# Kernel tuning notes

Measured on AMD Instinct MI355X. Metric: run time of the kernel, lower is better.

The kernel has to match this reference:

```python
import jax, jax.numpy as jnp
import numpy as np

B, S, D, H = 2, 2048, 1024, 16
HD = D // H  # head depth


def setup_inputs() -> dict:
    key = jax.random.key(0)
    ks = jax.random.split(key, 8)
    scale = 0.02
    K = jax.random.normal(ks[0], (B, S, D), jnp.float32)
    V = jax.random.normal(ks[1], (B, S, D), jnp.float32)
    Q = jax.random.normal(ks[2], (B, S, D), jnp.float32)
    # causal additive mask: 1.0 where attention is disallowed (strict upper triangle)
    mask = jnp.broadcast_to(
        jnp.triu(jnp.ones((S, S), jnp.float32), k=1)[None, None, :, :], (B, 1, S, S)
    )
    Wk = jax.random.normal(ks[3], (D, D), jnp.float32) * scale
    Wv = jax.random.normal(ks[4], (D, D), jnp.float32) * scale
    Wq = jax.random.normal(ks[5], (D, D), jnp.float32) * scale
    Wo = jax.random.normal(ks[6], (D, D), jnp.float32) * scale
    z = jnp.zeros((D,), jnp.float32)
    return {"K": K, "V": V, "Q": Q, "mask": mask,
            "Wk": Wk, "bk": z, "Wv": Wv, "bv": z,
            "Wq": Wq, "bq": z, "Wo": Wo, "bo": z}


def _split_heads(x):  # [B,S,D] -> [B,H,S,HD]
    return x.reshape(B, S, H, HD).transpose(0, 2, 1, 3)


def reference(K, V, Q, mask, Wk, bk, Wv, bv, Wq, bq, Wo, bo):
    k = _split_heads(K @ Wk + bk)
    v = _split_heads(V @ Wv + bv)
    q = _split_heads(Q @ Wq + bq)
    # NOTE: source scales by sqrt(d_model), not sqrt(head_depth)
    logits = jnp.einsum("bhqd,bhkd->bhqk", q, k) / jnp.sqrt(jnp.float32(D))
    logits = logits + mask * (-1e9)
    attn = jax.nn.softmax(logits, axis=-1)
    out = jnp.einsum("bhqk,bhkd->bhqd", attn, v)  # [B,H,S,HD]
    out = out.transpose(0, 2, 1, 3).reshape(B, S, D)
    return out @ Wo + bo
```

## Files before the change

### kernel.cpp

```cpp
#include <hip/hip_runtime.h>
#include <hip/hip_bf16.h>

typedef unsigned short u16;
typedef unsigned int u32;
typedef unsigned long long u64;
typedef __attribute__((ext_vector_type(8))) __bf16 bf16x8;
typedef __attribute__((ext_vector_type(4))) float f32x4;

#define SEQ 2048
#define DM 1024
#define NH 16
#define HDim 64

__device__ __forceinline__ float bf_lo(u32 u) { return __uint_as_float(u << 16); }
__device__ __forceinline__ float bf_hi(u32 u) { return __uint_as_float(u & 0xffff0000u); }
__device__ __forceinline__ u16 f2bf(float f) {
    u32 u = __float_as_uint(f);
    u32 r = (u + 0x7fffu + ((u >> 16) & 1u)) >> 16;
    return (u16)r;
}
__device__ __forceinline__ float bf2f(u16 h) { return __uint_as_float(((u32)h) << 16); }

#define GLD16(g, l)                                                         \
    __builtin_amdgcn_global_load_lds(                                       \
        (const __attribute__((address_space(1))) void*)(g),                 \
        (__attribute__((address_space(3))) void*)(l), 16, 0, 0)

__device__ __forceinline__ bool detect_f32(const u32* q)
{
    const u32 w = q[threadIdx.x & 63];
    const int e0 = ((w & 0xffffu) >> 7) & 0xff;
    const int e1 = (w >> 23) & 0xff;
    const unsigned long long b = __ballot(e0 >= 0x90 || e1 >= 0x90);
    return b != 0ull;
}

__global__ __launch_bounds__(256)
void prep_all(const void* __restrict__ Qin, const void* __restrict__ Kin,
              const void* __restrict__ Vin,
              const void* __restrict__ w0, const void* __restrict__ w1,
              const void* __restrict__ w2, const void* __restrict__ w3,
              const void* __restrict__ b0, const void* __restrict__ b1,
              const void* __restrict__ b2, const void* __restrict__ b3,
              u16* __restrict__ Xall, u16* __restrict__ Wtall,
              u16* __restrict__ ball)
{
    __shared__ u16 T[64 * 66];
    const bool f = detect_f32((const u32*)Qin);
    const int t = threadIdx.x;
    const int bid = blockIdx.x;

    if (bid < 6144) {
        const int z = bid >> 11;
        const int bx = bid & 2047;
        const void* src = (z == 0) ? Qin : (z == 1) ? Kin : Vin;
        const size_t i0 = ((size_t)bx * 256 + t) * 8;
        u16* d = Xall + (size_t)z * 4194304 + i0;
        if (f) {
            const uint4* s = reinterpret_cast<const uint4*>((const float*)src + i0);
            uint4 a = s[0], b = s[1];
            u16 o[8];
            o[0] = f2bf(__uint_as_float(a.x)); o[1] = f2bf(__uint_as_float(a.y));
            o[2] = f2bf(__uint_as_float(a.z)); o[3] = f2bf(__uint_as_float(a.w));
            o[4] = f2bf(__uint_as_float(b.x)); o[5] = f2bf(__uint_as_float(b.y));
            o[6] = f2bf(__uint_as_float(b.z)); o[7] = f2bf(__uint_as_float(b.w));
            *reinterpret_cast<uint4*>(d) = *reinterpret_cast<const uint4*>(o);
        } else {
            *reinterpret_cast<uint4*>(d) =
                *reinterpret_cast<const uint4*>((const u16*)src + i0);
        }
    } else if (bid < 7168) {
        const int r = bid - 6144;
        const int z = r >> 8;
        const void* src = (z == 0) ? w0 : (z == 1) ? w1 : (z == 2) ? w2 : w3;
        const int n0 = ((r >> 4) & 15) * 64;
        const int k0 = (r & 15) * 64;
        const int c = t & 63, g = t >> 6;
        if (f) {
            const float* W = (const float*)src;
#pragma unroll
            for (int i = 0; i < 16; i++) {
                const int kl = g * 16 + i;
                T[kl * 66 + c] = f2bf(W[(size_t)(k0 + kl) * DM + n0 + c]);
            }
        } else {
            const u16* W = (const u16*)src;
#pragma unroll
            for (int i = 0; i < 16; i++) {
                const int kl = g * 16 + i;
                T[kl * 66 + c] = W[(size_t)(k0 + kl) * DM + n0 + c];
            }
        }
        __syncthreads();
        u16* dst = Wtall + (size_t)z * 1048576;
#pragma unroll
        for (int i = 0; i < 16; i++) {
            const int nl = g * 16 + i;
            dst[(size_t)(n0 + nl) * DM + k0 + c] = T[c * 66 + nl];
        }
    } else {
#pragma unroll
        for (int j = 0; j < 16; j++) {
            const int idx = t * 16 + j;
            const int z = idx >> 10, e = idx & 1023;
            const void* src = (z == 0) ? b0 : (z == 1) ? b1 : (z == 2) ? b2 : b3;
            ball[idx] = f ? f2bf(((const float*)src)[e]) : ((const u16*)src)[e];
        }
    }
}

__global__ __launch_bounds__(256)
void gemm128(const u16* __restrict__ Xall, const u16* __restrict__ Wtall,
             const u16* __restrict__ ball, u16* __restrict__ Yall)
{
    __shared__ __align__(16) u16 As[128 * 32];
    __shared__ __align__(16) u16 Bs[128 * 32];

    const int zz = blockIdx.z;
    const bool swp = (zz != 2);
    const u16* X  = Xall + (size_t)zz * 4194304;
    const u16* Wt = Wtall + (size_t)zz * 1048576;

    const int t    = threadIdx.x;
    const int w    = t >> 6;
    const int lane = t & 63;
    const int quad = lane >> 4;
    const int ln   = lane & 15;
    const int m0   = blockIdx.y * 128;
    const int n0   = blockIdx.x * 128;

    f32x4 acc[4][4];
#pragma unroll
    for (int i = 0; i < 4; i++)
#pragma unroll
        for (int j = 0; j < 4; j++) acc[i][j] = (f32x4){0.f, 0.f, 0.f, 0.f};

    const u16* ag = X  + (size_t)(m0 + w * 32 + (lane >> 2)) * DM + (lane & 3) * 8;
    const u16* bg = Wt + (size_t)(n0 + w * 32 + (lane >> 2)) * DM + (lane & 3) * 8;
    u16* al = &As[w * 1024];
    u16* bl = &Bs[w * 1024];

    const int wr = (w >> 1) * 64;
    const int wc = (w & 1) * 64;

    for (int kk = 0; kk < DM; kk += 32) {
        GLD16(ag,           al);
        GLD16(ag + 16 * DM, al + 512);
        GLD16(bg,           bl);
        GLD16(bg + 16 * DM, bl + 512);
        ag += 32; bg += 32;
        __syncthreads();

        bf16x8 af[4], bfr[4];
#pragma unroll
        for (int rt = 0; rt < 4; rt++)
            af[rt] = *reinterpret_cast<const bf16x8*>(&As[(wr + rt * 16 + ln) * 32 + quad * 8]);
#pragma unroll
        for (int ct = 0; ct < 4; ct++)
            bfr[ct] = *reinterpret_cast<const bf16x8*>(&Bs[(wc + ct * 16 + ln) * 32 + quad * 8]);
        if (swp) {
#pragma unroll
            for (int rt = 0; rt < 4; rt++)
#pragma unroll
                for (int ct = 0; ct < 4; ct++)
                    acc[rt][ct] = __builtin_amdgcn_mfma_f32_16x16x32_bf16(
                        bfr[ct], af[rt], acc[rt][ct], 0, 0, 0);
        } else {
#pragma unroll
            for (int rt = 0; rt < 4; rt++)
#pragma unroll
                for (int ct = 0; ct < 4; ct++)
                    acc[rt][ct] = __builtin_amdgcn_mfma_f32_16x16x32_bf16(
                        af[rt], bfr[ct], acc[rt][ct], 0, 0, 0);
        }
        __syncthreads();
    }

    u16* Y = Yall + (size_t)zz * 4194304;

    if (swp) {
        const float scale = (zz == 0) ? 0.03125f : 1.0f;
#pragma unroll
        for (int ct = 0; ct < 4; ct++) {
            const int nb = n0 + wc + ct * 16 + quad * 4;
            const int h = nb >> 6, hd = nb & (HDim - 1);
            float bv[4];
#pragma unroll
            for (int r = 0; r < 4; r++) bv[r] = bf2f(ball[zz * 1024 + nb + r]);
#pragma unroll
            for (int rt = 0; rt < 4; rt++) {
                const int m = m0 + wr + rt * 16 + ln;
                const int b = m >> 11, s = m & (SEQ - 1);
                u16 o4[4];
#pragma unroll
                for (int r = 0; r < 4; r++)
                    o4[r] = f2bf((acc[rt][ct][r] + bv[r]) * scale);
                *reinterpret_cast<u64*>(
                    Y + (((size_t)(b * NH + h)) * SEQ + s) * HDim + hd) =
                    *reinterpret_cast<const u64*>(o4);
            }
        }
    } else {
#pragma unroll
        for (int ct = 0; ct < 4; ct++) {
            const int n = n0 + wc + ct * 16 + ln;
            const float bv = bf2f(ball[zz * 1024 + n]);
            const int h = n >> 6, hd = n & (HDim - 1);
#pragma unroll
            for (int rt = 0; rt < 4; rt++) {
                const int m = m0 + wr + rt * 16 + quad * 4;
                const int b = m >> 11, s = m & (SEQ - 1);
                u16 o4[4];
#pragma unroll
                for (int r = 0; r < 4; r++) o4[r] = f2bf(acc[rt][ct][r] + bv);
                *reinterpret_cast<u64*>(
                    Y + (((size_t)(b * NH + h) * HDim + hd) * SEQ + s)) =
                    *reinterpret_cast<const u64*>(o4);
            }
        }
    }
}

__device__ __forceinline__ void attn_tile2(
    const u16* __restrict__ Ks, const u16* __restrict__ Vs,
    u16* __restrict__ Ps, const bf16x8& qf0, const bf16x8& qf1,
    int kt, int qrow, int w, int quad, int ln, f32x4* o, float& l)
{
    f32x4 s[4];
#pragma unroll
    for (int ct = 0; ct < 4; ct++) {
        const u16* kr = &Ks[(ct * 16 + ln) * 72 + quad * 8];
        bf16x8 kf0 = *reinterpret_cast<const bf16x8*>(kr);
        bf16x8 kf1 = *reinterpret_cast<const bf16x8*>(kr + 32);
        f32x4 z = (f32x4){0.f, 0.f, 0.f, 0.f};
        z = __builtin_amdgcn_mfma_f32_16x16x32_bf16(kf0, qf0, z, 0, 0, 0);
        s[ct] = __builtin_amdgcn_mfma_f32_16x16x32_bf16(kf1, qf1, z, 0, 0, 0);
    }
#pragma unroll
    for (int ct = 0; ct < 4; ct++) {
        u16 o4[4];
#pragma unroll
        for (int r = 0; r < 4; r++) {
            const int kcol = kt * 64 + ct * 16 + quad * 4 + r;
            const float e = (kcol <= qrow) ? __expf(s[ct][r]) : 0.f;
            l += e;
            o4[r] = f2bf(e);
        }
        *reinterpret_cast<u64*>(&Ps[(w * 16 + ln) * 72 + ct * 16 + quad * 4]) =
            *reinterpret_cast<const u64*>(o4);
    }
#pragma unroll
    for (int ks = 0; ks < 2; ks++) {
        bf16x8 pf = *reinterpret_cast<const bf16x8*>(
            &Ps[(w * 16 + ln) * 72 + ks * 32 + quad * 8]);
#pragma unroll
        for (int nt = 0; nt < 4; nt++) {
            bf16x8 vf = *reinterpret_cast<const bf16x8*>(
                &Vs[(nt * 16 + ln) * 72 + ks * 32 + quad * 8]);
            o[nt] = __builtin_amdgcn_mfma_f32_16x16x32_bf16(pf, vf, o[nt], 0, 0, 0);
        }
    }
}

__global__ __launch_bounds__(256)
void attn_split(const u16* __restrict__ qh, const u16* __restrict__ kh,
                const u16* __restrict__ vt, u16* __restrict__ Opart,
                float* __restrict__ Lpart)
{
    __shared__ __align__(16) u16 Ks[64 * 72];
    __shared__ __align__(16) u16 Vs[64 * 72];
    __shared__ __align__(16) u16 Ps[64 * 72];

    const int t    = threadIdx.x;
    const int i    = blockIdx.x;
    const int bh   = blockIdx.y;
    const int c    = blockIdx.z;
    const int w    = t >> 6;
    const int lane = t & 63;
    const int quad = lane >> 4;
    const int ln   = lane & 15;
    const int qtH  = 31 - i;
    const int qtL  = i;
    const int m    = (i >= 8) ? 8 : 16 - i;
    const int kt0  = c ? m : 0;
    const int kt1  = c ? (qtH + 1) : m;

    const size_t kbase = (size_t)bh * SEQ * HDim;
    const size_t vbase = (size_t)bh * HDim * SEQ;

    const u16* qrH = qh + kbase + (size_t)(qtH * 64 + w * 16 + ln) * HDim;
    const bf16x8 qfH0 = *reinterpret_cast<const bf16x8*>(qrH + quad * 8);
    const bf16x8 qfH1 = *reinterpret_cast<const bf16x8*>(qrH + 32 + quad * 8);
    const u16* qrL = qh + kbase + (size_t)(qtL * 64 + w * 16 + ln) * HDim;
    const bf16x8 qfL0 = *reinterpret_cast<const bf16x8*>(qrL + quad * 8);
    const bf16x8 qfL1 = *reinterpret_cast<const bf16x8*>(qrL + 32 + quad * 8);

    f32x4 oH[4], oL[4];
    float lH = 0.f, lL = 0.f;
#pragma unroll
    for (int k = 0; k < 4; k++) {
        oH[k] = (f32x4){0.f, 0.f, 0.f, 0.f};
        oL[k] = (f32x4){0.f, 0.f, 0.f, 0.f};
    }

    const int srow = t >> 2;
    const int sc   = (t & 3) * 16;
    const int rowH = qtH * 64 + w * 16 + ln;
    const int rowL = qtL * 64 + w * 16 + ln;

    for (int kt = kt0; kt < kt1; kt++) {
        {
            const uint4* ks = reinterpret_cast<const uint4*>(
                kh + kbase + (size_t)(kt * 64 + srow) * HDim + sc);
            uint4* kd = reinterpret_cast<uint4*>(&Ks[srow * 72 + sc]);
            kd[0] = ks[0];
            kd[1] = ks[1];
            const uint4* vs = reinterpret_cast<const uint4*>(
                vt + vbase + (size_t)srow * SEQ + kt * 64 + sc);
            uint4* vd = reinterpret_cast<uint4*>(&Vs[srow * 72 + sc]);
            vd[0] = vs[0];
            vd[1] = vs[1];
        }
        __syncthreads();

        attn_tile2(Ks, Vs, Ps, qfH0, qfH1, kt, rowH, w, quad, ln, oH, lH);
        if (kt <= qtL)
            attn_tile2(Ks, Vs, Ps, qfL0, qfL1, kt, rowL, w, quad, ln, oL, lL);

        __syncthreads();
    }

    lH += __shfl_xor(lH, 16); lH += __shfl_xor(lH, 32);
    lL += __shfl_xor(lL, 16); lL += __shfl_xor(lL, 32);

    const size_t cb = ((size_t)c * 32 + bh) * SEQ;
    if (lane < 16) {
        Lpart[cb + qtH * 64 + w * 16 + lane] = lH;
        Lpart[cb + qtL * 64 + w * 16 + lane] = lL;
    }
#pragma unroll
    for (int r = 0; r < 4; r++) {
        const int rH = qtH * 64 + w * 16 + quad * 4 + r;
        const int rL = qtL * 64 + w * 16 + quad * 4 + r;
        u16* dH = Opart + (cb + rH) * HDim + ln;
        u16* dL = Opart + (cb + rL) * HDim + ln;
#pragma unroll
        for (int nt = 0; nt < 4; nt++) {
            dH[nt * 16] = f2bf(oH[nt][r]);
            dL[nt * 16] = f2bf(oL[nt][r]);
        }
    }
}

__global__ __launch_bounds__(256)
void attn_merge(const u16* __restrict__ Opart, const float* __restrict__ Lpart,
                u16* __restrict__ ctx)
{
    const size_t tid8 = (size_t)blockIdx.x * 256 + threadIdx.x;
    const int d8 = (int)(tid8 & 7);
    const int s  = (int)((tid8 >> 3) & (SEQ - 1));
    const int bh = (int)(tid8 >> 14);
    const size_t CSTR = (size_t)32 * SEQ * HDim;

    const uint4 a = *reinterpret_cast<const uint4*>(Opart + tid8 * 8);
    const uint4 b = *reinterpret_cast<const uint4*>(Opart + CSTR + tid8 * 8);
    const float l0 = Lpart[(size_t)bh * SEQ + s];
    const float l1 = Lpart[(size_t)32 * SEQ + (size_t)bh * SEQ + s];
    const float inv = 1.f / (l0 + l1);

    const u32 aw[4] = {a.x, a.y, a.z, a.w};
    const u32 bw[4] = {b.x, b.y, b.z, b.w};
    u32 ow[4];
#pragma unroll
    for (int p = 0; p < 4; p++) {
        const float lo = (bf_lo(aw[p]) + bf_lo(bw[p])) * inv;
        const float hi = (bf_hi(aw[p]) + bf_hi(bw[p])) * inv;
        ow[p] = (u32)f2bf(lo) | ((u32)f2bf(hi) << 16);
    }
    const int bb = bh >> 4, h = bh & 15;
    *reinterpret_cast<uint4*>(
        ctx + ((size_t)(bb * SEQ + s)) * DM + h * HDim + d8 * 8) =
        *reinterpret_cast<const uint4*>(ow);
}

__global__ __launch_bounds__(256)
void gemm_out(const u16* __restrict__ ctx, const u16* __restrict__ Wt,
              const u16* __restrict__ bias, void* __restrict__ dout,
              const u32* __restrict__ qdet)
{
    __shared__ __align__(16) u16 As[128 * 32];
    __shared__ __align__(16) u16 Bs[64 * 32];

    const int t    = threadIdx.x;
    const int w    = t >> 6;
    const int lane = t & 63;
    const int quad = lane >> 4;
    const int ln   = lane & 15;
    const int m0   = blockIdx.y * 128;
    const int n0   = blockIdx.x * 64;

    f32x4 acc[4][2];
#pragma unroll
    for (int i = 0; i < 4; i++)
#pragma unroll
        for (int j = 0; j < 2; j++) acc[i][j] = (f32x4){0.f, 0.f, 0.f, 0.f};

    const u16* ag = ctx + (size_t)(m0 + w * 32 + (lane >> 2)) * DM + (lane & 3) * 8;
    const u16* bg = Wt + (size_t)(n0 + w * 16 + (lane >> 2)) * DM + (lane & 3) * 8;
    u16* al = &As[w * 1024];
    u16* bl = &Bs[w * 512];

    const int wr = (w >> 1) * 64;
    const int wc = (w & 1) * 32;

    for (int kk = 0; kk < DM; kk += 32) {
        GLD16(ag,           al);
        GLD16(ag + 16 * DM, al + 512);
        GLD16(bg,           bl);
        ag += 32; bg += 32;
        __syncthreads();

        bf16x8 af[4], bfr[2];
#pragma unroll
        for (int rt = 0; rt < 4; rt++)
            af[rt] = *reinterpret_cast<const bf16x8*>(&As[(wr + rt * 16 + ln) * 32 + quad * 8]);
#pragma unroll
        for (int ct = 0; ct < 2; ct++)
            bfr[ct] = *reinterpret_cast<const bf16x8*>(&Bs[(wc + ct * 16 + ln) * 32 + quad * 8]);
#pragma unroll
        for (int rt = 0; rt < 4; rt++)
#pragma unroll
            for (int ct = 0; ct < 2; ct++)
                acc[rt][ct] = __builtin_amdgcn_mfma_f32_16x16x32_bf16(
                    af[rt], bfr[ct], acc[rt][ct], 0, 0, 0);
        __syncthreads();
    }

    const bool f = detect_f32(qdet);
#pragma unroll
    for (int ct = 0; ct < 2; ct++) {
        const int n = n0 + wc + ct * 16 + ln;
        const float bv = bf2f(bias[n]);
#pragma unroll
        for (int rt = 0; rt < 4; rt++) {
            const int mb = m0 + wr + rt * 16 + quad * 4;
#pragma unroll
            for (int r = 0; r < 4; r++) {
                const float val = acc[rt][ct][r] + bv;
                if (f) ((float*)dout)[(size_t)(mb + r) * DM + n] = val;
                else   ((u16*)dout)[(size_t)(mb + r) * DM + n] = f2bf(val);
            }
        }
    }
}

__global__ __launch_bounds__(64)
void detect_dtype(const u32* __restrict__ q, int* __restrict__ flag)
{
    const int t = threadIdx.x;
    const u32 w = q[t];
    const int e0 = ((w & 0xffffu) >> 7) & 0xff;
    const int e1 = (w >> 23) & 0xff;
    const unsigned long long b = __ballot(e0 >= 0x90 || e1 >= 0x90);
    if (t == 0) *flag = (b != 0ull) ? 1 : 0;
}

struct AttnAcc { f32x4 o[4]; float l[4]; };

__device__ __forceinline__ void attn_tile(
    const u16* __restrict__ Ks, const u16* __restrict__ Vs,
    u16* __restrict__ Ps, const bf16x8& qf0, const bf16x8& qf1,
    int kt, int rowb, int w, int quad, int ln, AttnAcc& a)
{
    f32x4 s[4];
#pragma unroll
    for (int ct = 0; ct < 4; ct++) {
        const u16* kr = &Ks[(ct * 16 + ln) * 72 + quad * 8];
        bf16x8 kf0 = *reinterpret_cast<const bf16x8*>(kr);
        bf16x8 kf1 = *reinterpret_cast<const bf16x8*>(kr + 32);
        f32x4 z = (f32x4){0.f, 0.f, 0.f, 0.f};
        z = __builtin_amdgcn_mfma_f32_16x16x32_bf16(qf0, kf0, z, 0, 0, 0);
        s[ct] = __builtin_amdgcn_mfma_f32_16x16x32_bf16(qf1, kf1, z, 0, 0, 0);
    }
#pragma unroll
    for (int ct = 0; ct < 4; ct++) {
        const int kcol = kt * 64 + ct * 16 + ln;
#pragma unroll
        for (int r = 0; r < 4; r++) {
            const float e = (kcol <= rowb + r) ? __expf(s[ct][r]) : 0.f;
            a.l[r] += e;
            Ps[(w * 16 + quad * 4 + r) * 68 + ct * 16 + ln] = f2bf(e);
        }
    }
#pragma unroll
    for (int ks = 0; ks < 2; ks++) {
        bf16x8 pf = *reinterpret_cast<const bf16x8*>(
            &Ps[(w * 16 + ln) * 68 + ks * 32 + quad * 8]);
#pragma unroll
        for (int nt = 0; nt < 4; nt++) {
            bf16x8 vf = *reinterpret_cast<const bf16x8*>(
                &Vs[(nt * 16 + ln) * 72 + ks * 32 + quad * 8]);
            a.o[nt] = __builtin_amdgcn_mfma_f32_16x16x32_bf16(pf, vf, a.o[nt], 0, 0, 0);
        }
    }
}

__global__ __launch_bounds__(256)
void attn_mfma(const u16* __restrict__ qh, const u16* __restrict__ kh,
               const u16* __restrict__ vt, u16* __restrict__ ctx)
{
    __shared__ __align__(16) u16 Ks[64 * 72];
    __shared__ __align__(16) u16 Vs[64 * 72];
    __shared__ __align__(16) u16 Ps[64 * 68];

    const int t    = threadIdx.x;
    const int i    = blockIdx.x;
    const int bh   = blockIdx.y;
    const int w    = t >> 6;
    const int lane = t & 63;
    const int quad = lane >> 4;
    const int ln   = lane & 15;
    const int qtH  = 31 - i;
    const int qtL  = i;

    const size_t kbase = (size_t)bh * SEQ * HDim;
    const size_t vbase = (size_t)bh * HDim * SEQ;

    const u16* qrH = qh + kbase + (size_t)(qtH * 64 + w * 16 + ln) * HDim;
    const bf16x8 qfH0 = *reinterpret_cast<const bf16x8*>(qrH + quad * 8);
    const bf16x8 qfH1 = *reinterpret_cast<const bf16x8*>(qrH + 32 + quad * 8);
    const u16* qrL = qh + kbase + (size_t)(qtL * 64 + w * 16 + ln) * HDim;
    const bf16x8 qfL0 = *reinterpret_cast<const bf16x8*>(qrL + quad * 8);
    const bf16x8 qfL1 = *reinterpret_cast<const bf16x8*>(qrL + 32 + quad * 8);

    AttnAcc aH, aL;
#pragma unroll
    for (int k = 0; k < 4; k++) {
        aH.o[k] = (f32x4){0.f, 0.f, 0.f, 0.f}; aH.l[k] = 0.f;
        aL.o[k] = (f32x4){0.f, 0.f, 0.f, 0.f}; aL.l[k] = 0.f;
    }

    const int srow = t >> 2;
    const int sc   = (t & 3) * 16;
    const int rowHb = qtH * 64 + w * 16 + quad * 4;
    const int rowLb = qtL * 64 + w * 16 + quad * 4;

    for (int kt = 0; kt <= qtH; kt++) {
        {
            const uint4* ks = reinterpret_cast<const uint4*>(
                kh + kbase + (size_t)(kt * 64 + srow) * HDim + sc);
            uint4* kd = reinterpret_cast<uint4*>(&Ks[srow * 72 + sc]);
            kd[0] = ks[0];
            kd[1] = ks[1];
            const uint4* vs = reinterpret_cast<const uint4*>(
                vt + vbase + (size_t)srow * SEQ + kt * 64 + sc);
            uint4* vd = reinterpret_cast<uint4*>(&Vs[srow * 72 + sc]);
            vd[0] = vs[0];
            vd[1] = vs[1];
        }
        __syncthreads();

        attn_tile(Ks, Vs, Ps, qfH0, qfH1, kt, rowHb, w, quad, ln, aH);
        if (kt <= qtL)
            attn_tile(Ks, Vs, Ps, qfL0, qfL1, kt, rowLb, w, quad, ln, aL);

        __syncthreads();
    }

#pragma unroll
    for (int m = 1; m < 16; m <<= 1) {
#pragma unroll
        for (int r = 0; r < 4; r++) {
            aH.l[r] += __shfl_xor(aH.l[r], m);
            aL.l[r] += __shfl_xor(aL.l[r], m);
        }
    }

    const int b = bh >> 4;
    const int h = bh & 15;
#pragma unroll
    for (int r = 0; r < 4; r++) {
        const float invH = 1.f / aH.l[r];
        const float invL = 1.f / aL.l[r];
        const int sH = qtH * 64 + w * 16 + quad * 4 + r;
        const int sL = qtL * 64 + w * 16 + quad * 4 + r;
        u16* dH = ctx + ((size_t)(b * SEQ + sH)) * DM + h * HDim + ln;
        u16* dL = ctx + ((size_t)(b * SEQ + sL)) * DM + h * HDim + ln;
#pragma unroll
        for (int nt = 0; nt < 4; nt++) {
            dH[nt * 16] = f2bf(aH.o[nt][r] * invH);
            dL[nt * 16] = f2bf(aL.o[nt][r] * invL);
        }
    }
}

__global__ __launch_bounds__(256)
void gemm_bias(const void* __restrict__ Xv, const void* __restrict__ Wv,
               const void* __restrict__ biasv, void* __restrict__ Yv,
               int M, int N, int K, int mode, int xsel, int wsel, int ysel,
               float scale, const int* __restrict__ flagp)
{
    __shared__ __align__(16) u16 As[64 * 32];
    __shared__ __align__(16) u16 Bs[64 * 40];

    const int f  = *flagp;
    const bool xf = (xsel != 0) && (f != 0);
    const bool wf = (wsel != 0) && (f != 0);
    const bool yf = (ysel != 0) && (f != 0);

    const u16*   Xb = (const u16*)Xv;
    const float* Xf = (const float*)Xv;
    const u16*   Wb = (const u16*)Wv;
    const float* Wf = (const float*)Wv;

    const int t    = threadIdx.x;
    const int m0   = blockIdx.y * 64;
    const int n0   = blockIdx.x * 64;
    const int w    = t >> 6;
    const int lane = t & 63;
    const int quad = lane >> 4;
    const int ln   = lane & 15;

    f32x4 acc[4];
#pragma unroll
    for (int i = 0; i < 4; i++) acc[i] = (f32x4){0.f, 0.f, 0.f, 0.f};

    const int a_row = t >> 2;
    const int a_c8  = (t & 3) * 8;
    const int b_n   = t & 63;
    const int b_k8  = (t >> 6) * 8;

    for (int kk = 0; kk < K; kk += 32) {
        const size_t aoff = (size_t)(m0 + a_row) * K + kk + a_c8;
        if (!xf) {
            *reinterpret_cast<uint4*>(&As[a_row * 32 + a_c8]) =
                *reinterpret_cast<const uint4*>(Xb + aoff);
        } else {
            const float* src = Xf + aoff;
            uint4 u0 = reinterpret_cast<const uint4*>(src)[0];
            uint4 u1 = reinterpret_cast<const uint4*>(src)[1];
            u16 tmp[8];
            tmp[0] = f2bf(__uint_as_float(u0.x));
            tmp[1] = f2bf(__uint_as_float(u0.y));
            tmp[2] = f2bf(__uint_as_float(u0.z));
            tmp[3] = f2bf(__uint_as_float(u0.w));
            tmp[4] = f2bf(__uint_as_float(u1.x));
            tmp[5] = f2bf(__uint_as_float(u1.y));
            tmp[6] = f2bf(__uint_as_float(u1.z));
            tmp[7] = f2bf(__uint_as_float(u1.w));
            *reinterpret_cast<uint4*>(&As[a_row * 32 + a_c8]) =
                *reinterpret_cast<const uint4*>(tmp);
        }
        u16 tmp[8];
        if (!wf) {
#pragma unroll
            for (int j = 0; j < 8; j++)
                tmp[j] = Wb[(size_t)(kk + b_k8 + j) * N + n0 + b_n];
        } else {
#pragma unroll
            for (int j = 0; j < 8; j++)
                tmp[j] = f2bf(Wf[(size_t)(kk + b_k8 + j) * N + n0 + b_n]);
        }
        *reinterpret_cast<uint4*>(&Bs[b_n * 40 + b_k8]) =
            *reinterpret_cast<const uint4*>(tmp);

        __syncthreads();

        bf16x8 bfrag = *reinterpret_cast<const bf16x8*>(&Bs[(w * 16 + ln) * 40 + quad * 8]);
#pragma unroll
        for (int rt = 0; rt < 4; rt++) {
            bf16x8 afrag = *reinterpret_cast<const bf16x8*>(&As[(rt * 16 + ln) * 32 + quad * 8]);
            acc[rt] = __builtin_amdgcn_mfma_f32_16x16x32_bf16(afrag, bfrag, acc[rt], 0, 0, 0);
        }
        __syncthreads();
    }

    const int n = n0 + w * 16 + ln;
    const float bv = wf ? ((const float*)biasv)[n] : bf2f(((const u16*)biasv)[n]);
#pragma unroll
    for (int rt = 0; rt < 4; rt++) {
        if (mode == 2) {
            const int m = m0 + rt * 16 + quad * 4;
            const int b = m >> 11;
            const int s = m & (SEQ - 1);
            const int h = n >> 6;
            const int hd = n & (HDim - 1);
            u16 o4[4];
#pragma unroll
            for (int r = 0; r < 4; r++) o4[r] = f2bf((acc[rt][r] + bv) * scale);
            *reinterpret_cast<u64*>(
                (u16*)Yv + (((size_t)(b * NH + h) * HDim + hd) * SEQ + s)) =
                *reinterpret_cast<const u64*>(o4);
        } else {
#pragma unroll
            for (int r = 0; r < 4; r++) {
                const int m = m0 + rt * 16 + quad * 4 + r;
                const float val = (acc[rt][r] + bv) * scale;
                if (mode == 0) {
                    if (yf) ((float*)Yv)[(size_t)m * N + n] = val;
                    else    ((u16*)Yv)[(size_t)m * N + n] = f2bf(val);
                } else {
                    const int b = m >> 11;
                    const int s = m & (SEQ - 1);
                    const int h = n >> 6;
                    const int hd = n & (HDim - 1);
                    ((u16*)Yv)[(((size_t)(b * NH + h)) * SEQ + s) * HDim + hd] = f2bf(val);
                }
            }
        }
    }
}

extern "C" void kernel_launch(void* const* d_in, const int* in_sizes, int n_in,
                              void* d_out, int out_size, void* d_ws, size_t ws_size,
                              hipStream_t stream)
{
    const void* Kin = d_in[0];
    const void* Vin = d_in[1];
    const void* Qin = d_in[2];
    const void* Wk = d_in[4];
    const void* bk = d_in[5];
    const void* Wv = d_in[6];
    const void* bv = d_in[7];
    const void* Wq = d_in[8];
    const void* bq = d_in[9];
    const void* Wo = d_in[10];
    const void* bo = d_in[11];

    char* ws = (char*)d_ws;
    const size_t NEED = ((size_t)29360128 + 4096) * 2 + 256;

    if (ws_size >= NEED) {
        u16* Xall  = (u16*)ws;
        u16* Yall  = (u16*)ws + 12582912;
        u16* Wtall = (u16*)ws + 25165824;
        u16* ball  = (u16*)ws + 29360128;
        u16* qhp   = Yall;
        u16* khp   = Yall + 4194304;
        u16* vtp   = Yall + 8388608;
        u16* ctx   = Xall;
        u16* Opart = Xall + 4194304;
        float* Lpart = (float*)Wtall;

        hipLaunchKernelGGL(prep_all, dim3(7169), dim3(256), 0, stream,
                           Qin, Kin, Vin, Wq, Wk, Wv, Wo, bq, bk, bv, bo,
                           Xall, Wtall, ball);

        hipLaunchKernelGGL(gemm128, dim3(8, 32, 3), dim3(256), 0, stream,
                           Xall, Wtall, ball, Yall);

        hipLaunchKernelGGL(attn_split, dim3(16, 32, 2), dim3(256), 0, stream,
                           qhp, khp, vtp, Opart, Lpart);

        hipLaunchKernelGGL(attn_merge, dim3(2048), dim3(256), 0, stream,
                           Opart, Lpart, ctx);

        hipLaunchKernelGGL(gemm_out, dim3(16, 32), dim3(256), 0, stream,
                           ctx, Wtall + (size_t)3 * 1048576, ball + 3 * 1024,
                           d_out, (const u32*)Qin);
    } else {
        const size_t SEG = (size_t)2 * SEQ * DM * sizeof(u16);
        u16* qh  = (u16*)(ws);
        u16* khd = (u16*)(ws + SEG);
        u16* vtd = (u16*)(ws + 2 * SEG);
        u16* ctx = (u16*)(ws + 3 * SEG);
        int* flag = (int*)(ws + 4 * SEG);

        hipLaunchKernelGGL(detect_dtype, dim3(1), dim3(64), 0, stream,
                           (const u32*)Qin, flag);

        const int M = 2 * SEQ;
        dim3 ggrid(DM / 64, M / 64);
        dim3 gblk(256);

        hipLaunchKernelGGL(gemm_bias, ggrid, gblk, 0, stream, Qin, Wq, bq, qh,  M, DM, DM, 1, 1, 1, 0, 0.03125f, flag);
        hipLaunchKernelGGL(gemm_bias, ggrid, gblk, 0, stream, Kin, Wk, bk, khd, M, DM, DM, 1, 1, 1, 0, 1.0f,     flag);
        hipLaunchKernelGGL(gemm_bias, ggrid, gblk, 0, stream, Vin, Wv, bv, vtd, M, DM, DM, 2, 1, 1, 0, 1.0f,     flag);

        hipLaunchKernelGGL(attn_mfma, dim3(16, 2 * NH), dim3(256), 0,
                           stream, qh, khd, vtd, ctx);

        hipLaunchKernelGGL(gemm_bias, ggrid, gblk, 0, stream, ctx, Wo, bo, d_out, M, DM, DM, 0, 0, 1, 1, 1.0f, flag);
    }
}
```

Before: 269.9 us.

## Double-buffer GEMM LDS tiles with XOR swizzle and prefetch attention K/V tiles

Both projection GEMMs and the output GEMM now use two LDS buffers, so the global-to-LDS load of the next K-slice is issued before computing on the current one, leaving one barrier per step instead of two. The global source columns and LDS read offsets are XOR-swizzled to reduce LDS bank conflicts on the fragment reads. The attention kernel prefetches the next K/V tile into registers while computing the current tile. The cost is doubled LDS use in the GEMMs and extra registers in attention, which may lower occupancy.

```diff
diff --git a/kernel.cpp b/kernel.cpp
--- a/kernel.cpp
+++ b/kernel.cpp
@@ -113,8 +113,8 @@
 void gemm128(const u16* __restrict__ Xall, const u16* __restrict__ Wtall,
              const u16* __restrict__ ball, u16* __restrict__ Yall)
 {
-    __shared__ __align__(16) u16 As[128 * 32];
-    __shared__ __align__(16) u16 Bs[128 * 32];
+    __shared__ __align__(16) u16 As[2][128 * 32];
+    __shared__ __align__(16) u16 Bs[2][128 * 32];
 
     const int zz = blockIdx.z;
     const bool swp = (zz != 2);
@@ -135,46 +135,56 @@
 #pragma unroll
         for (int j = 0; j < 4; j++) acc[i][j] = (f32x4){0.f, 0.f, 0.f, 0.f};
 
-    const u16* ag = X  + (size_t)(m0 + w * 32 + (lane >> 2)) * DM + (lane & 3) * 8;
-    const u16* bg = Wt + (size_t)(n0 + w * 32 + (lane >> 2)) * DM + (lane & 3) * 8;
-    u16* al = &As[w * 1024];
-    u16* bl = &Bs[w * 1024];
+    const int swz = (lane >> 3) & 3;
+    const u16* ag = X  + (size_t)(m0 + w * 32 + (lane >> 2)) * DM + ((lane & 3) ^ swz) * 8;
+    const u16* bg = Wt + (size_t)(n0 + w * 32 + (lane >> 2)) * DM + ((lane & 3) ^ swz) * 8;
 
     const int wr = (w >> 1) * 64;
     const int wc = (w & 1) * 64;
-
-    for (int kk = 0; kk < DM; kk += 32) {
-        GLD16(ag,           al);
-        GLD16(ag + 16 * DM, al + 512);
-        GLD16(bg,           bl);
-        GLD16(bg + 16 * DM, bl + 512);
-        ag += 32; bg += 32;
-        __syncthreads();
-
-        bf16x8 af[4], bfr[4];
-#pragma unroll
-        for (int rt = 0; rt < 4; rt++)
-            af[rt] = *reinterpret_cast<const bf16x8*>(&As[(wr + rt * 16 + ln) * 32 + quad * 8]);
-#pragma unroll
-        for (int ct = 0; ct < 4; ct++)
-            bfr[ct] = *reinterpret_cast<const bf16x8*>(&Bs[(wc + ct * 16 + ln) * 32 + quad * 8]);
-        if (swp) {
-#pragma unroll
-            for (int rt = 0; rt < 4; rt++)
-#pragma unroll
-                for (int ct = 0; ct < 4; ct++)
-                    acc[rt][ct] = __builtin_amdgcn_mfma_f32_16x16x32_bf16(
-                        bfr[ct], af[rt], acc[rt][ct], 0, 0, 0);
-        } else {
-#pragma unroll
-            for (int rt = 0; rt < 4; rt++)
-#pragma unroll
-                for (int ct = 0; ct < 4; ct++)
-                    acc[rt][ct] = __builtin_amdgcn_mfma_f32_16x16x32_bf16(
-                        af[rt], bfr[ct], acc[rt][ct], 0, 0, 0);
-        }
-        __syncthreads();
-    }
+    const int rs = (quad ^ ((ln >> 1) & 3)) * 8;
+
+#define GSTAGE(B)                                        \
+    {                                                    \
+        GLD16(ag,           &As[B][w * 1024]);           \
+        GLD16(ag + 16 * DM, &As[B][w * 1024 + 512]);     \
+        GLD16(bg,           &Bs[B][w * 1024]);           \
+        GLD16(bg + 16 * DM, &Bs[B][w * 1024 + 512]);     \
+        ag += 32; bg += 32;                              \
+    }
+
+#define GCOMP(B)                                                              \
+    {                                                                         \
+        bf16x8 af[4], bfr[4];                                                 \
+        _Pragma("unroll") for (int rt = 0; rt < 4; rt++)                      \
+            af[rt] = *reinterpret_cast<const bf16x8*>(                        \
+                &As[B][(wr + rt * 16 + ln) * 32 + rs]);                       \
+        _Pragma("unroll") for (int ct = 0; ct < 4; ct++)                      \
+            bfr[ct] = *reinterpret_cast<const bf16x8*>(                       \
+                &Bs[B][(wc + ct * 16 + ln) * 32 + rs]);                       \
+        if (swp) {                                                            \
+            _Pragma("unroll") for (int rt = 0; rt < 4; rt++)                  \
+                _Pragma("unroll") for (int ct = 0; ct < 4; ct++)              \
+                    acc[rt][ct] = __builtin_amdgcn_mfma_f32_16x16x32_bf16(    \
+                        bfr[ct], af[rt], acc[rt][ct], 0, 0, 0);               \
+        } else {                                                              \
+            _Pragma("unroll") for (int rt = 0; rt < 4; rt++)                  \
+                _Pragma("unroll") for (int ct = 0; ct < 4; ct++)              \
+                    acc[rt][ct] = __builtin_amdgcn_mfma_f32_16x16x32_bf16(    \
+                        af[rt], bfr[ct], acc[rt][ct], 0, 0, 0);               \
+        }                                                                     \
+    }
+
+    GSTAGE(0);
+    __syncthreads();
+#pragma unroll 1
+    for (int it = 0; it < 15; ++it) {
+        GSTAGE(1); GCOMP(0); __syncthreads();
+        GSTAGE(0); GCOMP(1); __syncthreads();
+    }
+    GSTAGE(1); GCOMP(0); __syncthreads();
+    GCOMP(1);
+#undef GSTAGE
+#undef GCOMP
 
     u16* Y = Yall + (size_t)zz * 4194304;
 
@@ -308,20 +318,34 @@
     const int rowH = qtH * 64 + w * 16 + ln;
     const int rowL = qtL * 64 + w * 16 + ln;
 
+    uint4 kr0, kr1, vr0, vr1;
+    {
+        const uint4* ksp = reinterpret_cast<const uint4*>(
+            kh + kbase + (size_t)(kt0 * 64 + srow) * HDim + sc);
+        kr0 = ksp[0]; kr1 = ksp[1];
+        const uint4* vsp = reinterpret_cast<const uint4*>(
+            vt + vbase + (size_t)srow * SEQ + kt0 * 64 + sc);
+        vr0 = vsp[0]; vr1 = vsp[1];
+    }
+
     for (int kt = kt0; kt < kt1; kt++) {
         {
-            const uint4* ks = reinterpret_cast<const uint4*>(
-                kh + kbase + (size_t)(kt * 64 + srow) * HDim + sc);
             uint4* kd = reinterpret_cast<uint4*>(&Ks[srow * 72 + sc]);
-            kd[0] = ks[0];
-            kd[1] = ks[1];
-            const uint4* vs = reinterpret_cast<const uint4*>(
-                vt + vbase + (size_t)srow * SEQ + kt * 64 + sc);
+            kd[0] = kr0; kd[1] = kr1;
             uint4* vd = reinterpret_cast<uint4*>(&Vs[srow * 72 + sc]);
-            vd[0] = vs[0];
-            vd[1] = vs[1];
+            vd[0] = vr0; vd[1] = vr1;
         }
         __syncthreads();
+
+        if (kt + 1 < kt1) {
+            const uint4* ksp = reinterpret_cast<const uint4*>(
+                kh + kbase + (size_t)((kt + 1) * 64 + srow) * HDim + sc);
+            kr0 = ksp[0]; kr1 = ksp[1];
+            const uint4* vsp = reinterpret_cast<const uint4*>(
+                vt + vbase + (size_t)srow * SEQ + (kt + 1) * 64 + sc);
+            vr0 = vsp[0]; vr1 = vsp[1];
+            __builtin_amdgcn_sched_barrier(0);
+        }
 
         attn_tile2(Ks, Vs, Ps, qfH0, qfH1, kt, rowH, w, quad, ln, oH, lH);
         if (kt <= qtL)
@@ -388,8 +412,8 @@
               const u16* __restrict__ bias, void* __restrict__ dout,
               const u32* __restrict__ qdet)
 {
-    __shared__ __align__(16) u16 As[128 * 32];
-    __shared__ __align__(16) u16 Bs[64 * 32];
+    __shared__ __align__(16) u16 As[2][128 * 32];
+    __shared__ __align__(16) u16 Bs[2][64 * 32];
 
     const int t    = threadIdx.x;
     const int w    = t >> 6;
@@ -405,36 +429,48 @@
 #pragma unroll
         for (int j = 0; j < 2; j++) acc[i][j] = (f32x4){0.f, 0.f, 0.f, 0.f};
 
-    const u16* ag = ctx + (size_t)(m0 + w * 32 + (lane >> 2)) * DM + (lane & 3) * 8;
-    const u16* bg = Wt + (size_t)(n0 + w * 16 + (lane >> 2)) * DM + (lane & 3) * 8;
-    u16* al = &As[w * 1024];
-    u16* bl = &Bs[w * 512];
+    const int swz = (lane >> 3) & 3;
+    const u16* ag = ctx + (size_t)(m0 + w * 32 + (lane >> 2)) * DM + ((lane & 3) ^ swz) * 8;
+    const u16* bg = Wt + (size_t)(n0 + w * 16 + (lane >> 2)) * DM + ((lane & 3) ^ swz) * 8;
 
     const int wr = (w >> 1) * 64;
     const int wc = (w & 1) * 32;
-
-    for (int kk = 0; kk < DM; kk += 32) {
-        GLD16(ag,           al);
-        GLD16(ag + 16 * DM, al + 512);
-        GLD16(bg,           bl);
-        ag += 32; bg += 32;
-        __syncthreads();
-
-        bf16x8 af[4], bfr[2];
-#pragma unroll
-        for (int rt = 0; rt < 4; rt++)
-            af[rt] = *reinterpret_cast<const bf16x8*>(&As[(wr + rt * 16 + ln) * 32 + quad * 8]);
-#pragma unroll
-        for (int ct = 0; ct < 2; ct++)
-            bfr[ct] = *reinterpret_cast<const bf16x8*>(&Bs[(wc + ct * 16 + ln) * 32 + quad * 8]);
-#pragma unroll
-        for (int rt = 0; rt < 4; rt++)
-#pragma unroll
-            for (int ct = 0; ct < 2; ct++)
-                acc[rt][ct] = __builtin_amdgcn_mfma_f32_16x16x32_bf16(
-                    af[rt], bfr[ct], acc[rt][ct], 0, 0, 0);
-        __syncthreads();
-    }
+    const int rs = (quad ^ ((ln >> 1) & 3)) * 8;
+
+#define OSTAGE(B)                                        \
+    {                                                    \
+        GLD16(ag,           &As[B][w * 1024]);           \
+        GLD16(ag + 16 * DM, &As[B][w * 1024 + 512]);     \
+        GLD16(bg,           &Bs[B][w * 512]);            \
+        ag += 32; bg += 32;                              \
+    }
+
+#define OCOMP(B)                                                              \
+    {                                                                         \
+        bf16x8 af[4], bfr[2];                                                 \
+        _Pragma("unroll") for (int rt = 0; rt < 4; rt++)                      \
+            af[rt] = *reinterpret_cast<const bf16x8*>(                        \
+                &As[B][(wr + rt * 16 + ln) * 32 + rs]);                       \
+        _Pragma("unroll") for (int ct = 0; ct < 2; ct++)                      \
+            bfr[ct] = *reinterpret_cast<const bf16x8*>(                       \
+                &Bs[B][(wc + ct * 16 + ln) * 32 + rs]);                       \
+        _Pragma("unroll") for (int rt = 0; rt < 4; rt++)                      \
+            _Pragma("unroll") for (int ct = 0; ct < 2; ct++)                  \
+                acc[rt][ct] = __builtin_amdgcn_mfma_f32_16x16x32_bf16(        \
+                    af[rt], bfr[ct], acc[rt][ct], 0, 0, 0);                   \
+    }
+
+    OSTAGE(0);
+    __syncthreads();
+#pragma unroll 1
+    for (int it = 0; it < 15; ++it) {
+        OSTAGE(1); OCOMP(0); __syncthreads();
+        OSTAGE(0); OCOMP(1); __syncthreads();
+    }
+    OSTAGE(1); OCOMP(0); __syncthreads();
+    OCOMP(1);
+#undef OSTAGE
+#undef OCOMP
 
     const bool f = detect_f32(qdet);
 #pragma unroll
```

Result: faster. 263.5 us (-2.3%).
